# Performance work log

Hardware: AMD Instinct MI355X
Metric: run time of the kernel (lower is better)

## Reference

```python
import jax, jax.numpy as jnp
import numpy as np

NUM_HEADS = 16
HIDDEN = 1024
ATTN_DIM = 64            # per-head q/k dim
HEAD_OUT = 64            # per-head v dim
OUT_DIM = 1024
BATCH, SEQ = 2, 2048


def setup_inputs() -> dict:
    key = jax.random.key(0)
    ks = jax.random.split(key, 9)
    s_in = 1.0 / np.sqrt(HIDDEN)
    s_o = 1.0 / np.sqrt(NUM_HEADS * HEAD_OUT)
    return {
        "x": jax.random.normal(ks[0], (BATCH, SEQ, HIDDEN), dtype=jnp.float32),
        # Linear weights stored [in, out] so y = x @ W + b
        "Wq": jax.random.uniform(ks[1], (HIDDEN, NUM_HEADS * ATTN_DIM), jnp.float32, -s_in, s_in),
        "bq": jax.random.uniform(ks[2], (NUM_HEADS * ATTN_DIM,), jnp.float32, -s_in, s_in),
        "Wk": jax.random.uniform(ks[3], (HIDDEN, NUM_HEADS * ATTN_DIM), jnp.float32, -s_in, s_in),
        "bk": jax.random.uniform(ks[4], (NUM_HEADS * ATTN_DIM,), jnp.float32, -s_in, s_in),
        "Wv": jax.random.uniform(ks[5], (HIDDEN, NUM_HEADS * HEAD_OUT), jnp.float32, -s_in, s_in),
        "bv": jax.random.uniform(ks[6], (HIDDEN, NUM_HEADS * HEAD_OUT)[1:], jnp.float32, -s_in, s_in),
        "Wo": jax.random.uniform(ks[7], (NUM_HEADS * HEAD_OUT, OUT_DIM), jnp.float32, -s_o, s_o),
        "bo": jax.random.uniform(ks[8], (OUT_DIM,), jnp.float32, -s_o, s_o),
    }


def _split_heads(y, h):
    b, s, _ = y.shape
    return y.reshape(b, s, h, -1).transpose(0, 2, 1, 3)  # [b, h, s, d]


def reference(x, Wq, bq, Wk, bk, Wv, bv, Wo, bo):
    h = NUM_HEADS
    q = _split_heads(x @ Wq + bq, h)                    # [b,h,s,dq]
    k = _split_heads(x @ Wk + bk, h)                    # [b,h,s,dq]
    v = _split_heads(x @ Wv + bv, h)                    # [b,h,s,dv]
    scale = 1.0 / jnp.sqrt(jnp.float32(ATTN_DIM))
    # pattern[b,h,i,j] = key_i . query_j  (i=key index, j=query index)
    pattern = jnp.einsum('bhid,bhjd->bhij', k, q) * scale
    # softmax over key axis (dim=-2), matching t.softmax(..., dim=-2)
    prob = jax.nn.softmax(pattern, axis=-2)             # [b,h,key,query]
    # out[b,h,s,d] = sum_i prob[b,h,i,s] * v[b,h,i,d]
    out = jnp.einsum('bhis,bhid->bhsd', prob, v)        # [b,h,s,dv]
    b, _, s, dv = out.shape
    concat = out.transpose(0, 2, 1, 3).reshape(b, s, h * dv)
    return concat @ Wo + bo
```

## Files before the change

kernel.cpp:

```cpp
#include <hip/hip_runtime.h>
#include <cstdint>
#include <cstddef>

using f16   = _Float16;
using f16x4 = __attribute__((ext_vector_type(4))) _Float16;
using f16x8 = __attribute__((ext_vector_type(8))) _Float16;
using f32x4 = __attribute__((ext_vector_type(4))) float;

__device__ __forceinline__ f32x4 mfma16(f16x8 a, f16x8 b, f32x4 c) {
  return __builtin_amdgcn_mfma_f32_16x16x32_f16(a, b, c, 0, 0, 0);
}

__device__ __forceinline__ void gld16(const f16* g, f16* l) {
  __builtin_amdgcn_global_load_lds(
      (__attribute__((address_space(1))) void*)g,
      (__attribute__((address_space(3))) void*)l, 16, 0, 0);
}

constexpr int BATCH = 2, SEQL = 2048, HID = 1024, NH = 16, DH = 64;
constexpr int TOK = BATCH * SEQL;
constexpr int NQKV = 3 * HID;

__global__ __launch_bounds__(256) void k_convert_x(const float* __restrict__ x,
                                                   f16* __restrict__ xh) {
  int i = (blockIdx.x * 256 + threadIdx.x) * 4;
  float4 v = *(const float4*)(x + i);
  f16x4 o = { (f16)v.x, (f16)v.y, (f16)v.z, (f16)v.w };
  *(f16x4*)(xh + i) = o;
}

__global__ __launch_bounds__(256) void k_transpose(const float* __restrict__ Wq,
                                                   const float* __restrict__ Wk,
                                                   const float* __restrict__ Wv,
                                                   const float* __restrict__ Wo,
                                                   f16* __restrict__ WT,
                                                   f16* __restrict__ WoT) {
  __shared__ float tile[32][33];
  int mat = blockIdx.z;
  const float* W = (mat == 0) ? Wq : (mat == 1) ? Wk : (mat == 2) ? Wv : Wo;
  int in0 = blockIdx.x * 32, out0 = blockIdx.y * 32;
  int c = threadIdx.x & 31, r8 = threadIdx.x >> 5;
#pragma unroll
  for (int i = 0; i < 4; i++) {
    int r = r8 + i * 8;
    tile[r][c] = W[(size_t)(in0 + r) * HID + out0 + c];
  }
  __syncthreads();
#pragma unroll
  for (int i = 0; i < 4; i++) {
    int r = r8 + i * 8;
    f16 v = (f16)tile[c][r];
    if (mat == 3) WoT[(size_t)(out0 + r) * HID + in0 + c] = v;
    else          WT[(size_t)(mat * HID + out0 + r) * HID + in0 + c] = v;
  }
}

__global__ __launch_bounds__(256, 2) void k_gemm_qkv(
    const f16* __restrict__ xh, const f16* __restrict__ WT,
    const float* __restrict__ bq, const float* __restrict__ bk,
    const float* __restrict__ bv,
    f16* __restrict__ Qh, f16* __restrict__ Kh, f16* __restrict__ Vp) {
  constexpr int K = HID;
  int m0 = blockIdx.x * 128, n0 = blockIdx.y * 128;
  int tid = threadIdx.x;
  int w = tid >> 6, lane = tid & 63, lr = lane & 15, lq = lane >> 4;
  int wm = w >> 1, wn = w & 1;
  __shared__ f16 Ash[128 * 32];
  __shared__ f16 Bsh[128 * 32];
  f32x4 acc[4][4];
#pragma unroll
  for (int i = 0; i < 4; i++)
#pragma unroll
    for (int j = 0; j < 4; j++) acc[i][j] = (f32x4){0.f, 0.f, 0.f, 0.f};

  int row0 = tid >> 2, seg0 = tid & 3;
  int row1 = (256 + tid) >> 2;
  const f16* Ag0 = xh + (size_t)(m0 + row0) * K + seg0 * 8;
  const f16* Ag1 = xh + (size_t)(m0 + row1) * K + seg0 * 8;
  const f16* Bg0 = WT + (size_t)(n0 + row0) * K + seg0 * 8;
  const f16* Bg1 = WT + (size_t)(n0 + row1) * K + seg0 * 8;

  for (int k0 = 0; k0 < K; k0 += 32) {
    __syncthreads();
    gld16(Ag0 + k0, Ash + tid * 8);
    gld16(Ag1 + k0, Ash + (256 + tid) * 8);
    gld16(Bg0 + k0, Bsh + tid * 8);
    gld16(Bg1 + k0, Bsh + (256 + tid) * 8);
    __syncthreads();
    f16x8 af[4], bfr[4];
#pragma unroll
    for (int mt = 0; mt < 4; mt++)
      af[mt] = *(const f16x8*)(Ash + (wm * 64 + mt * 16 + lr) * 32 + lq * 8);
#pragma unroll
    for (int nt = 0; nt < 4; nt++)
      bfr[nt] = *(const f16x8*)(Bsh + (wn * 64 + nt * 16 + lr) * 32 + lq * 8);
#pragma unroll
    for (int mt = 0; mt < 4; mt++)
#pragma unroll
      for (int nt = 0; nt < 4; nt++)
        acc[mt][nt] = mfma16(af[mt], bfr[nt], acc[mt][nt]);
  }

#pragma unroll
  for (int nt = 0; nt < 4; nt++) {
    int o = n0 + wn * 64 + nt * 16 + lr;
    int sec = o >> 10, o1 = o & 1023, hh = o1 >> 6, dd = o1 & 63;
    float bias = (sec == 0) ? bq[o1] : (sec == 1) ? bk[o1] : bv[o1];
#pragma unroll
    for (int mt = 0; mt < 4; mt++) {
      int t0 = m0 + wm * 64 + mt * 16 + lq * 4;
      int b = t0 >> 11, s0 = t0 & (SEQL - 1);
      size_t bh = (size_t)(b * NH + hh);
      if (sec == 2) {
        f16x4 pv = { (f16)(acc[mt][nt][0] + bias), (f16)(acc[mt][nt][1] + bias),
                     (f16)(acc[mt][nt][2] + bias), (f16)(acc[mt][nt][3] + bias) };
        int pb = (s0 & ~31) | ((s0 & 12) << 1) | ((s0 >> 2) & 4);
        *(f16x4*)(Vp + (bh * DH + dd) * SEQL + pb) = pv;
      } else {
        f16* dst = (sec == 0) ? Qh : Kh;
#pragma unroll
        for (int r = 0; r < 4; r++)
          dst[(bh * SEQL + s0 + r) * DH + dd] = (f16)(acc[mt][nt][r] + bias);
      }
    }
  }
}

__global__ __launch_bounds__(256, 2) void k_attn(const f16* __restrict__ Qh,
                                                 const f16* __restrict__ Kh,
                                                 const f16* __restrict__ Vp,
                                                 f16* __restrict__ Ao) {
  int bh = blockIdx.x;
  int qblk = blockIdx.y;
  int b = bh >> 4, h = bh & 15;
  int tid = threadIdx.x, w = tid >> 6, lane = tid & 63, lr = lane & 15, lq = lane >> 4;

  __shared__ f16 Ksh[2][64 * 72];
  __shared__ f16 Vsh[2][64 * 72];

  f16x8 qf[2][2];
#pragma unroll
  for (int qt = 0; qt < 2; qt++) {
    const f16* Qbase =
        Qh + ((size_t)bh * SEQL + qblk * 128 + w * 32 + qt * 16 + lr) * DH;
#pragma unroll
    for (int ks = 0; ks < 2; ks++) {
      qf[qt][ks] = *(const f16x8*)(Qbase + ks * 32 + lq * 8);
      qf[qt][ks] = qf[qt][ks] * (f16)0.18033688f;
    }
  }

  f32x4 O[2][4];
#pragma unroll
  for (int qt = 0; qt < 2; qt++)
#pragma unroll
    for (int dt = 0; dt < 4; dt++) O[qt][dt] = (f32x4){0.f, 0.f, 0.f, 0.f};
  float lsum[2] = {0.f, 0.f};

  int srow = tid >> 3, sseg = tid & 7, srow1 = srow + 32;
  const f16* Kg0 = Kh + ((size_t)bh * SEQL + srow) * DH + sseg * 8;
  const f16* Kg1 = Kh + ((size_t)bh * SEQL + srow1) * DH + sseg * 8;
  const f16* Vg0 = Vp + ((size_t)bh * DH + srow) * SEQL + sseg * 8;
  const f16* Vg1 = Vp + ((size_t)bh * DH + srow1) * SEQL + sseg * 8;

  uint4 kr0 = *(const uint4*)(Kg0), kr1 = *(const uint4*)(Kg1);
  uint4 vr0 = *(const uint4*)(Vg0), vr1 = *(const uint4*)(Vg1);

  for (int kb = 0; kb < SEQL / 64; kb++) {
    f16* Kp = Ksh[kb & 1];
    f16* Vq = Vsh[kb & 1];
    *(uint4*)(Kp + srow * 72 + sseg * 8) = kr0;
    *(uint4*)(Kp + srow1 * 72 + sseg * 8) = kr1;
    *(uint4*)(Vq + srow * 72 + sseg * 8) = vr0;
    *(uint4*)(Vq + srow1 * 72 + sseg * 8) = vr1;
    if (kb < SEQL / 64 - 1) {
      size_t ko = (size_t)(kb + 1) * 64 * DH;
      int vo = (kb + 1) * 64;
      kr0 = *(const uint4*)(Kg0 + ko);
      kr1 = *(const uint4*)(Kg1 + ko);
      vr0 = *(const uint4*)(Vg0 + vo);
      vr1 = *(const uint4*)(Vg1 + vo);
    }
    __syncthreads();

    f32x4 sacc[2][4];
#pragma unroll
    for (int qt = 0; qt < 2; qt++)
#pragma unroll
      for (int kt = 0; kt < 4; kt++) sacc[qt][kt] = (f32x4){0.f, 0.f, 0.f, 0.f};
#pragma unroll
    for (int ks = 0; ks < 2; ks++) {
#pragma unroll
      for (int kt = 0; kt < 4; kt++) {
        f16x8 kf = *(const f16x8*)(Kp + (kt * 16 + lr) * 72 + ks * 32 + lq * 8);
        sacc[0][kt] = mfma16(kf, qf[0][ks], sacc[0][kt]);
        sacc[1][kt] = mfma16(kf, qf[1][ks], sacc[1][kt]);
      }
    }

    f16x8 pf[2][2];
#pragma unroll
    for (int qt = 0; qt < 2; qt++) {
      float part = 0.f;
#pragma unroll
      for (int kt = 0; kt < 4; kt++) {
        float p0 = __builtin_amdgcn_exp2f(sacc[qt][kt][0]);
        float p1 = __builtin_amdgcn_exp2f(sacc[qt][kt][1]);
        float p2 = __builtin_amdgcn_exp2f(sacc[qt][kt][2]);
        float p3 = __builtin_amdgcn_exp2f(sacc[qt][kt][3]);
        part += (p0 + p1) + (p2 + p3);
        int s = kt >> 1, off = (kt & 1) * 4;
        pf[qt][s][off + 0] = (f16)p0; pf[qt][s][off + 1] = (f16)p1;
        pf[qt][s][off + 2] = (f16)p2; pf[qt][s][off + 3] = (f16)p3;
      }
      lsum[qt] += part;
    }

#pragma unroll
    for (int s = 0; s < 2; s++) {
#pragma unroll
      for (int dt = 0; dt < 4; dt++) {
        f16x8 vf = *(const f16x8*)(Vq + (dt * 16 + lr) * 72 + s * 32 + lq * 8);
        O[0][dt] = mfma16(vf, pf[0][s], O[0][dt]);
        O[1][dt] = mfma16(vf, pf[1][s], O[1][dt]);
      }
    }
  }

#pragma unroll
  for (int qt = 0; qt < 2; qt++) {
    float l1 = lsum[qt] + __shfl_xor(lsum[qt], 16);
    float ltot = l1 + __shfl_xor(l1, 32);
    float inv = 1.0f / ltot;
    int q = qblk * 128 + w * 32 + qt * 16 + lr;
    f16* dst = Ao + ((size_t)b * SEQL + q) * HID + h * DH;
#pragma unroll
    for (int dt = 0; dt < 4; dt++) {
      f16x4 o = { (f16)(O[qt][dt][0] * inv), (f16)(O[qt][dt][1] * inv),
                  (f16)(O[qt][dt][2] * inv), (f16)(O[qt][dt][3] * inv) };
      *(f16x4*)(dst + dt * 16 + lq * 4) = o;
    }
  }
}

__global__ __launch_bounds__(256, 2) void k_gemm_out(const f16* __restrict__ Ah,
                                                     const f16* __restrict__ WoT,
                                                     const float* __restrict__ bo,
                                                     float* __restrict__ out) {
  constexpr int K = HID;
  int m0 = blockIdx.x * 128, n0 = blockIdx.y * 64;
  int tid = threadIdx.x;
  int w = tid >> 6, lane = tid & 63, lr = lane & 15, lq = lane >> 4;
  int wm = w >> 1, wn = w & 1;
  __shared__ f16 Ash[128 * 32];
  __shared__ f16 Bsh[64 * 32];
  f32x4 acc[4][2];
#pragma unroll
  for (int i = 0; i < 4; i++)
#pragma unroll
    for (int j = 0; j < 2; j++) acc[i][j] = (f32x4){0.f, 0.f, 0.f, 0.f};

  int row0 = tid >> 2, seg0 = tid & 3;
  int row1 = (256 + tid) >> 2;
  const f16* Ag0 = Ah + (size_t)(m0 + row0) * K + seg0 * 8;
  const f16* Ag1 = Ah + (size_t)(m0 + row1) * K + seg0 * 8;
  const f16* Bg0 = WoT + (size_t)(n0 + row0) * K + seg0 * 8;

  for (int k0 = 0; k0 < K; k0 += 32) {
    __syncthreads();
    gld16(Ag0 + k0, Ash + tid * 8);
    gld16(Ag1 + k0, Ash + (256 + tid) * 8);
    gld16(Bg0 + k0, Bsh + tid * 8);
    __syncthreads();
    f16x8 af[4], bfr[2];
#pragma unroll
    for (int mt = 0; mt < 4; mt++)
      af[mt] = *(const f16x8*)(Ash + (wm * 64 + mt * 16 + lr) * 32 + lq * 8);
#pragma unroll
    for (int nt = 0; nt < 2; nt++)
      bfr[nt] = *(const f16x8*)(Bsh + (wn * 32 + nt * 16 + lr) * 32 + lq * 8);
#pragma unroll
    for (int mt = 0; mt < 4; mt++)
#pragma unroll
      for (int nt = 0; nt < 2; nt++)
        acc[mt][nt] = mfma16(af[mt], bfr[nt], acc[mt][nt]);
  }

#pragma unroll
  for (int nt = 0; nt < 2; nt++) {
    int o = n0 + wn * 32 + nt * 16 + lr;
    float bias = bo[o];
#pragma unroll
    for (int mt = 0; mt < 4; mt++) {
      int t0 = m0 + wm * 64 + mt * 16 + lq * 4;
#pragma unroll
      for (int r = 0; r < 4; r++)
        out[(size_t)(t0 + r) * HID + o] = acc[mt][nt][r] + bias;
    }
  }
}

extern "C" void kernel_launch(void* const* d_in, const int* in_sizes, int n_in,
                              void* d_out, int out_size, void* d_ws, size_t ws_size,
                              hipStream_t stream) {
  const float* x  = (const float*)d_in[0];
  const float* Wq = (const float*)d_in[1];
  const float* bq = (const float*)d_in[2];
  const float* Wk = (const float*)d_in[3];
  const float* bk = (const float*)d_in[4];
  const float* Wv = (const float*)d_in[5];
  const float* bv = (const float*)d_in[6];
  const float* Wo = (const float*)d_in[7];
  const float* bo = (const float*)d_in[8];

  char* ws = (char*)d_ws;
  f16* xh  = (f16*)(ws + 0);
  f16* WT  = (f16*)(ws + 8388608);
  f16* WoT = (f16*)(ws + 14680064);
  f16* Qh  = (f16*)(ws + 16777216);
  f16* Kh  = (f16*)(ws + 25165824);
  f16* Vp  = (f16*)(ws + 33554432);
  f16* Ao  = (f16*)(ws + 41943040);

  k_convert_x<<<TOK * HID / 1024, 256, 0, stream>>>(x, xh);
  k_transpose<<<dim3(32, 32, 4), 256, 0, stream>>>(Wq, Wk, Wv, Wo, WT, WoT);
  k_gemm_qkv<<<dim3(TOK / 128, NQKV / 128), 256, 0, stream>>>(xh, WT, bq, bk, bv,
                                                              Qh, Kh, Vp);
  k_attn<<<dim3(BATCH * NH, SEQL / 128), 256, 0, stream>>>(Qh, Kh, Vp, Ao);
  k_gemm_out<<<dim3(TOK / 128, HID / 64), 256, 0, stream>>>(Ao, WoT, bo,
                                                            (float*)d_out);
}
```

Baseline: 187.7 us.

## Split attention over two key halves and merge partial sums in a new kernel

The attention grid is doubled by giving each block half of the key sequence. Each block writes an unnormalized fp16 partial output and a row-sum to workspace buffers reused from earlier stages. A new merge kernel adds the two partials and normalizes them. This raises block count and occupancy (launch bounds also raised for qkv and attention), at the cost of extra global traffic, a launch, and a precision risk from storing unnormalized fp16 sums.

```diff
diff --git a/kernel.cpp b/kernel.cpp
--- a/kernel.cpp
+++ b/kernel.cpp
@@ -55,7 +55,7 @@
   }
 }
 
-__global__ __launch_bounds__(256, 2) void k_gemm_qkv(
+__global__ __launch_bounds__(256, 3) void k_gemm_qkv(
     const f16* __restrict__ xh, const f16* __restrict__ WT,
     const float* __restrict__ bq, const float* __restrict__ bk,
     const float* __restrict__ bv,
@@ -126,12 +126,16 @@
   }
 }
 
-__global__ __launch_bounds__(256, 2) void k_attn(const f16* __restrict__ Qh,
+__global__ __launch_bounds__(256, 4) void k_attn(const f16* __restrict__ Qh,
                                                  const f16* __restrict__ Kh,
                                                  const f16* __restrict__ Vp,
-                                                 f16* __restrict__ Ao) {
+                                                 f16* __restrict__ Op0,
+                                                 f16* __restrict__ Op1,
+                                                 float* __restrict__ Lw) {
   int bh = blockIdx.x;
-  int qblk = blockIdx.y;
+  int qblk = blockIdx.y & 15;
+  int split = blockIdx.y >> 4;
+  int kb0 = split * 16;
   int b = bh >> 4, h = bh & 15;
   int tid = threadIdx.x, w = tid >> 6, lane = tid & 63, lr = lane & 15, lq = lane >> 4;
 
@@ -158,22 +162,22 @@
   float lsum[2] = {0.f, 0.f};
 
   int srow = tid >> 3, sseg = tid & 7, srow1 = srow + 32;
-  const f16* Kg0 = Kh + ((size_t)bh * SEQL + srow) * DH + sseg * 8;
-  const f16* Kg1 = Kh + ((size_t)bh * SEQL + srow1) * DH + sseg * 8;
-  const f16* Vg0 = Vp + ((size_t)bh * DH + srow) * SEQL + sseg * 8;
-  const f16* Vg1 = Vp + ((size_t)bh * DH + srow1) * SEQL + sseg * 8;
+  const f16* Kg0 = Kh + ((size_t)bh * SEQL + kb0 * 64 + srow) * DH + sseg * 8;
+  const f16* Kg1 = Kh + ((size_t)bh * SEQL + kb0 * 64 + srow1) * DH + sseg * 8;
+  const f16* Vg0 = Vp + ((size_t)bh * DH + srow) * SEQL + kb0 * 64 + sseg * 8;
+  const f16* Vg1 = Vp + ((size_t)bh * DH + srow1) * SEQL + kb0 * 64 + sseg * 8;
 
   uint4 kr0 = *(const uint4*)(Kg0), kr1 = *(const uint4*)(Kg1);
   uint4 vr0 = *(const uint4*)(Vg0), vr1 = *(const uint4*)(Vg1);
 
-  for (int kb = 0; kb < SEQL / 64; kb++) {
+  for (int kb = 0; kb < 16; kb++) {
     f16* Kp = Ksh[kb & 1];
     f16* Vq = Vsh[kb & 1];
     *(uint4*)(Kp + srow * 72 + sseg * 8) = kr0;
     *(uint4*)(Kp + srow1 * 72 + sseg * 8) = kr1;
     *(uint4*)(Vq + srow * 72 + sseg * 8) = vr0;
     *(uint4*)(Vq + srow1 * 72 + sseg * 8) = vr1;
-    if (kb < SEQL / 64 - 1) {
+    if (kb < 15) {
       size_t ko = (size_t)(kb + 1) * 64 * DH;
       int vo = (kb + 1) * 64;
       kr0 = *(const uint4*)(Kg0 + ko);
@@ -227,20 +231,37 @@
     }
   }
 
+  f16* Op = split ? Op1 : Op0;
 #pragma unroll
   for (int qt = 0; qt < 2; qt++) {
     float l1 = lsum[qt] + __shfl_xor(lsum[qt], 16);
     float ltot = l1 + __shfl_xor(l1, 32);
-    float inv = 1.0f / ltot;
     int q = qblk * 128 + w * 32 + qt * 16 + lr;
-    f16* dst = Ao + ((size_t)b * SEQL + q) * HID + h * DH;
+    if (lq == 0) Lw[split * (32 * 2048) + bh * 2048 + q] = ltot;
+    f16* dst = Op + ((size_t)b * SEQL + q) * HID + h * DH;
 #pragma unroll
     for (int dt = 0; dt < 4; dt++) {
-      f16x4 o = { (f16)(O[qt][dt][0] * inv), (f16)(O[qt][dt][1] * inv),
-                  (f16)(O[qt][dt][2] * inv), (f16)(O[qt][dt][3] * inv) };
+      f16x4 o = { (f16)O[qt][dt][0], (f16)O[qt][dt][1],
+                  (f16)O[qt][dt][2], (f16)O[qt][dt][3] };
       *(f16x4*)(dst + dt * 16 + lq * 4) = o;
     }
   }
+}
+
+__global__ __launch_bounds__(256) void k_merge(const f16* __restrict__ Op0,
+                                               f16* __restrict__ Ao,
+                                               const float* __restrict__ Lw) {
+  int i = (blockIdx.x * 256 + threadIdx.x) * 4;
+  int b = i >> 21, s = (i >> 10) & 2047, h = (i & 1023) >> 6;
+  int li = (b * 16 + h) * 2048 + s;
+  float inv = 1.0f / (Lw[li] + Lw[32 * 2048 + li]);
+  f16x4 a = *(const f16x4*)(Op0 + i);
+  f16x4 c = *(const f16x4*)(Ao + i);
+  f16x4 o = { (f16)(((float)a[0] + (float)c[0]) * inv),
+              (f16)(((float)a[1] + (float)c[1]) * inv),
+              (f16)(((float)a[2] + (float)c[2]) * inv),
+              (f16)(((float)a[3] + (float)c[3]) * inv) };
+  *(f16x4*)(Ao + i) = o;
 }
 
 __global__ __launch_bounds__(256, 2) void k_gemm_out(const f16* __restrict__ Ah,
@@ -314,19 +335,22 @@
   const float* bo = (const float*)d_in[8];
 
   char* ws = (char*)d_ws;
-  f16* xh  = (f16*)(ws + 0);
-  f16* WT  = (f16*)(ws + 8388608);
-  f16* WoT = (f16*)(ws + 14680064);
-  f16* Qh  = (f16*)(ws + 16777216);
-  f16* Kh  = (f16*)(ws + 25165824);
-  f16* Vp  = (f16*)(ws + 33554432);
-  f16* Ao  = (f16*)(ws + 41943040);
+  f16*   xh  = (f16*)(ws + 0);
+  f16*   Op0 = (f16*)(ws + 0);
+  f16*   WT  = (f16*)(ws + 8388608);
+  float* Lw  = (float*)(ws + 8388608);
+  f16*   WoT = (f16*)(ws + 14680064);
+  f16*   Qh  = (f16*)(ws + 16777216);
+  f16*   Kh  = (f16*)(ws + 25165824);
+  f16*   Vp  = (f16*)(ws + 33554432);
+  f16*   Ao  = (f16*)(ws + 41943040);
 
   k_convert_x<<<TOK * HID / 1024, 256, 0, stream>>>(x, xh);
   k_transpose<<<dim3(32, 32, 4), 256, 0, stream>>>(Wq, Wk, Wv, Wo, WT, WoT);
   k_gemm_qkv<<<dim3(TOK / 128, NQKV / 128), 256, 0, stream>>>(xh, WT, bq, bk, bv,
                                                               Qh, Kh, Vp);
-  k_attn<<<dim3(BATCH * NH, SEQL / 128), 256, 0, stream>>>(Qh, Kh, Vp, Ao);
+  k_attn<<<dim3(BATCH * NH, 32), 256, 0, stream>>>(Qh, Kh, Vp, Op0, Ao, Lw);
+  k_merge<<<TOK * HID / 1024, 256, 0, stream>>>(Op0, Ao, Lw);
   k_gemm_out<<<dim3(TOK / 128, HID / 64), 256, 0, stream>>>(Ao, WoT, bo,
                                                             (float*)d_out);
 }
```

Result: slower. 195.5 us (+4.1%).
